# Kernel tuning notes

Hardware: AMD Instinct MI355X
Metric: run time of the kernel (lower is better)

The kernel has to match this reference:

```python
import jax, jax.numpy as jnp
import numpy as np

C_IN = 5
KERNEL = 4
DEPTH = 4
C = C_IN + 3  # original + time + 2 CNN channels


def conv1d(x, w, b):
    # x: (B, Cin, L), w: (Cout, Cin, K) -> (B, Cout, L-K+1), 'VALID' padding as in signatory.Augment defaults
    y = jax.lax.conv_general_dilated(x, w, (1,), 'VALID',
                                     dimension_numbers=('NCH', 'OIH', 'NCH'))
    return y + b[None, :, None]


def augment(inp, w1, b1, w2, b2, w3, b3):
    # inp: (B, L, C_in). Mirrors signatory.Augment with layer_sizes=(8,8,2), kernel_size=4,
    # include_original=True, include_time=True, activation=relu (between layers, not after last).
    B, L, _ = inp.shape
    trunc = KERNEL - 1
    orig = inp[:, trunc:, :]                                   # (B, L-3, C_in)
    time = jnp.linspace(0.0, 1.0, L, dtype=inp.dtype)[trunc:]  # time over original stream, truncated
    time = jnp.broadcast_to(time[None, :, None], (B, L - trunc, 1))
    h = conv1d(inp.transpose(0, 2, 1), w1, b1)   # (B, 8, L-3)
    h = conv1d(jax.nn.relu(h), w2, b2)           # (B, 8, L-3)
    h = conv1d(jax.nn.relu(h), w3, b3)           # (B, 2, L-3)
    return jnp.concatenate([orig, time, h.transpose(0, 2, 1)], axis=2)  # (B, L-3, C)


def signature(path):
    # Truncated path signature, depth 4, basepoint=True (zero basepoint prepended).
    # Chen's relation: sig <- sig (tensor) exp(dx), maintained as per-level tensors.
    B, S, Cc = path.shape
    base = jnp.zeros((B, 1, Cc), path.dtype)
    inc = jnp.diff(jnp.concatenate([base, path], axis=1), axis=1)  # (B, S, C) increments incl. basepoint
    inc = inc.transpose(1, 0, 2)  # (S, B, C) for scan

    def step(carry, dx):
        s1, s2, s3, s4 = carry
        # exp(dx) levels: dx^(k)/k!
        e1 = dx
        e2 = jnp.einsum('bi,bj->bij', dx, dx) / 2.0
        e3 = jnp.einsum('bij,bk->bijk', e2, dx) / 3.0
        e4 = jnp.einsum('bijk,bl->bijkl', e3, dx) / 4.0
        # Chen: (A (x) B)_k = sum_i A_i (x) B_{k-i}, A_0 = B_0 = 1
        n1 = s1 + e1
        n2 = s2 + e2 + jnp.einsum('bi,bj->bij', s1, e1)
        n3 = (s3 + e3 + jnp.einsum('bi,bjk->bijk', s1, e2)
              + jnp.einsum('bij,bk->bijk', s2, e1))
        n4 = (s4 + e4 + jnp.einsum('bi,bjkl->bijkl', s1, e3)
              + jnp.einsum('bij,bkl->bijkl', s2, e2)
              + jnp.einsum('bijk,bl->bijkl', s3, e1))
        return (n1, n2, n3, n4), None

    init = (jnp.zeros((B, Cc), path.dtype),
            jnp.zeros((B, Cc, Cc), path.dtype),
            jnp.zeros((B, Cc, Cc, Cc), path.dtype),
            jnp.zeros((B, Cc, Cc, Cc, Cc), path.dtype))
    (s1, s2, s3, s4), _ = jax.lax.scan(step, init, inc)
    return jnp.concatenate([s1.reshape(B, -1), s2.reshape(B, -1),
                            s3.reshape(B, -1), s4.reshape(B, -1)], axis=1)  # (B, 4680)


def setup_inputs() -> dict:
    key = jax.random.key(0)
    ks = jax.random.split(key, 4)
    B, L = 64, 256

    def init_conv(k, cout, cin, ksz):
        bound = 1.0 / np.sqrt(cin * ksz)
        kw, kb = jax.random.split(k)
        w = jax.random.uniform(kw, (cout, cin, ksz), jnp.float32, -bound, bound)
        b = jax.random.uniform(kb, (cout,), jnp.float32, -bound, bound)
        return w, b

    w1, b1 = init_conv(ks[1], 8, C_IN, KERNEL)
    w2, b2 = init_conv(ks[2], 8, 8, 1)
    w3, b3 = init_conv(ks[3], 2, 8, 1)
    inp = jax.random.normal(ks[0], (B, L, C_IN), jnp.float32)
    return {"inp": inp, "w1": w1, "b1": b1, "w2": w2, "b2": b2, "w3": w3, "b3": b3}


def reference(inp, w1, b1, w2, b2, w3, b3):
    x = augment(inp, w1, b1, w2, b2, w3, b3)  # (B, L-3, C)
    return signature(x)                       # (B, 4680)
```

## Files before the change

### kernel.cpp

```cpp
#include <hip/hip_runtime.h>

#define L_IN  256
#define CIN   5
#define SIG_N 4680

__global__ __launch_bounds__(512) void sig_fused_kernel(
    const float* __restrict__ inp,
    const float* __restrict__ w1, const float* __restrict__ b1,
    const float* __restrict__ w2, const float* __restrict__ b2,
    const float* __restrict__ w3, const float* __restrict__ b3,
    float* __restrict__ out)
{
    const int blk  = blockIdx.x;
    const int b    = blk >> 2;
    const int iq   = blk & 3;
    const int i0   = 2 * iq;
    const int tid  = threadIdx.x;
    const int w    = tid >> 6;
    const int lane = tid & 63;
    const int j    = lane >> 3;
    const int k    = lane & 7;

    __shared__ __align__(16) float dxs[264][8];
    __shared__ __align__(16) float sig3[8][592];
    __shared__ __align__(16) float s4red[8][1024];

    auto PI = [&](int x) {
        return (((x >> 1) == 0) | ((x >> 1) == iq)) ? (x ^ i0) : x;
    };

    const float* __restrict__ x = inp + b * (L_IN * CIN);
    float o[8];
    if (tid < 253) {
        float h1[8];
        #pragma unroll
        for (int q = 0; q < 8; ++q) h1[q] = b1[q];
        #pragma unroll
        for (int kk = 0; kk < 4; ++kk) {
            #pragma unroll
            for (int ci = 0; ci < CIN; ++ci) {
                float v = x[(tid + kk) * CIN + ci];
                #pragma unroll
                for (int q = 0; q < 8; ++q) h1[q] = fmaf(v, w1[q * 20 + ci * 4 + kk], h1[q]);
            }
        }
        float r1v[8];
        #pragma unroll
        for (int q = 0; q < 8; ++q) r1v[q] = h1[q] > 0.f ? h1[q] : 0.f;
        float h2[8];
        #pragma unroll
        for (int q = 0; q < 8; ++q) h2[q] = b2[q];
        #pragma unroll
        for (int p = 0; p < 8; ++p) {
            #pragma unroll
            for (int q = 0; q < 8; ++q) h2[q] = fmaf(r1v[p], w2[q * 8 + p], h2[q]);
        }
        float r2v[8];
        #pragma unroll
        for (int q = 0; q < 8; ++q) r2v[q] = h2[q] > 0.f ? h2[q] : 0.f;
        float h30 = b3[0], h31 = b3[1];
        #pragma unroll
        for (int p = 0; p < 8; ++p) {
            h30 = fmaf(r2v[p], w3[p], h30);
            h31 = fmaf(r2v[p], w3[8 + p], h31);
        }
        #pragma unroll
        for (int cc = 0; cc < 5; ++cc) o[cc] = x[(tid + 3) * CIN + cc];
        o[5] = (float)(tid + 3) * (1.0f / 255.0f);
        o[6] = h30;
        o[7] = h31;
    }
    if (tid < 88) dxs[253 + (tid >> 3)][tid & 7] = 0.f;
    if (tid < 253) {
        #pragma unroll
        for (int c = 0; c < 8; ++c) dxs[tid][PI(c)] = o[c];
    }
    __syncthreads();
    float curr[8], prevr[8];
    if (tid < 253) {
        #pragma unroll
        for (int ch = 0; ch < 8; ++ch) {
            curr[ch]  = dxs[tid][ch];
            prevr[ch] = (tid > 0) ? dxs[tid - 1][ch] : 0.f;
        }
    }
    __syncthreads();
    if (tid < 253) {
        #pragma unroll
        for (int ch = 0; ch < 8; ++ch) dxs[tid][ch] = curr[ch] - prevr[ch];
    }
    __syncthreads();

    const int rbase = w * 32;
    float t1[8], t2r[8], t3r[8];
    float s4v[2][8];
    #pragma unroll
    for (int i = 0; i < 8; ++i) { t1[i] = 0.f; t2r[i] = 0.f; t3r[i] = 0.f; }
    #pragma unroll
    for (int m = 0; m < 2; ++m)
        #pragma unroll
        for (int l = 0; l < 8; ++l) s4v[m][l] = 0.f;

    const float4* __restrict__ dx4 = reinterpret_cast<const float4*>(&dxs[0][0]);
    float own_p[2], bb_p[2];
    float4 r0_p[2], r1_p[2];
    #pragma unroll
    for (int u = 0; u < 2; ++u) {
        own_p[u] = dxs[rbase + u][k];
        bb_p[u]  = dxs[rbase + u][j];
        r0_p[u]  = dx4[2 * (rbase + u)];
        r1_p[u]  = dx4[2 * (rbase + u) + 1];
    }

    for (int tb = 0; tb < 32; tb += 2) {
        #pragma unroll
        for (int u = 0; u < 2; ++u) {
            const int tn = rbase + tb + u + 2;
            float  own_n = dxs[tn][k];
            float  bb_n  = dxs[tn][j];
            float4 r0_n  = dx4[2 * tn];
            float4 r1_n  = dx4[2 * tn + 1];

            const float own = own_p[u];
            const float bb  = bb_p[u];
            const float4 r0 = r0_p[u];
            const float4 r1 = r1_p[u];
            const float rr[8] = { r0.x, r0.y, r0.z, r0.w, r1.x, r1.y, r1.z, r1.w };

            const float c4_0 = fmaf(own, fmaf(bb, fmaf(t1[0], (1.0f / 6.0f),
                                r0.x * (1.0f / 24.0f)), 0.5f * t2r[0]), t3r[0]);
            const float c4_1 = fmaf(own, fmaf(bb, fmaf(t1[1], (1.0f / 6.0f),
                                r0.y * (1.0f / 24.0f)), 0.5f * t2r[1]), t3r[1]);
            #pragma unroll
            for (int l = 0; l < 8; ++l) {
                s4v[0][l] = fmaf(c4_0, rr[l], s4v[0][l]);
                s4v[1][l] = fmaf(c4_1, rr[l], s4v[1][l]);
            }

            #pragma unroll
            for (int i = 0; i < 8; ++i) {
                const float a  = rr[i];
                const float c3 = fmaf(bb, fmaf(t1[i], 0.5f, a * (1.0f / 6.0f)), t2r[i]);
                t3r[i] = fmaf(c3, own, t3r[i]);
                t2r[i] = fmaf(fmaf(a, 0.5f, t1[i]), bb, t2r[i]);
                t1[i] += a;
            }

            own_p[u] = own_n; bb_p[u] = bb_n;
            r0_p[u] = r0_n;   r1_p[u] = r1_n;
        }
    }

    if (lane == 0) {
        #pragma unroll
        for (int i = 0; i < 8; ++i) sig3[w][i] = t1[i];
    }
    if (k == 0) {
        #pragma unroll
        for (int i = 0; i < 8; ++i) sig3[w][8 + i * 8 + j] = t2r[i];
    }
    #pragma unroll
    for (int i = 0; i < 8; ++i) sig3[w][72 + (i * 8 + j) * 8 + k] = t3r[i];
    __syncthreads();

    float p1[2] = {0.f, 0.f}, p2[2] = {0.f, 0.f}, p3[2] = {0.f, 0.f};

    auto combine = [&](int cc) {
        const float* __restrict__ lp = sig3[cc];
        const float s1j  = lp[j];
        const float s1k  = lp[k];
        const float s2jk = lp[8 + j * 8 + k];
        #pragma unroll
        for (int m = 0; m < 2; ++m) {
            const float s1i  = lp[m];
            const float s2ij = lp[8 + m * 8 + j];
            const float s3i  = lp[72 + (m * 8 + j) * 8 + k];
            const float np3 = p3[m] + s3i + p1[m] * s2jk + p2[m] * s1k;
            const float np2 = p2[m] + s2ij + p1[m] * s1j;
            p3[m] = np3; p2[m] = np2; p1[m] += s1i;
        }
    };

    for (int cc = 0; cc < w; ++cc) combine(cc);
    {
        const float* __restrict__ lp = sig3[w];
        const float4 s1a = *reinterpret_cast<const float4*>(lp);
        const float4 s1b = *reinterpret_cast<const float4*>(lp + 4);
        const float4 s2a = *reinterpret_cast<const float4*>(lp + 8 + k * 8);
        const float4 s2b = *reinterpret_cast<const float4*>(lp + 8 + k * 8 + 4);
        const float4 s3a = *reinterpret_cast<const float4*>(lp + 72 + (j * 8 + k) * 8);
        const float4 s3b = *reinterpret_cast<const float4*>(lp + 72 + (j * 8 + k) * 8 + 4);
        const float s1r[8] = { s1a.x, s1a.y, s1a.z, s1a.w, s1b.x, s1b.y, s1b.z, s1b.w };
        const float s2r[8] = { s2a.x, s2a.y, s2a.z, s2a.w, s2b.x, s2b.y, s2b.z, s2b.w };
        const float s3r[8] = { s3a.x, s3a.y, s3a.z, s3a.w, s3b.x, s3b.y, s3b.z, s3b.w };
        #pragma unroll
        for (int m = 0; m < 2; ++m)
            #pragma unroll
            for (int l = 0; l < 8; ++l)
                s4v[m][l] = fmaf(p1[m], s3r[l],
                             fmaf(p2[m], s2r[l],
                              fmaf(p3[m], s1r[l], s4v[m][l])));
    }

    float* __restrict__ ob = out + (size_t)b * SIG_N;
    if (w == 7) {
        combine(7);
        const int pj = PI(j);
        const int pk = PI(k);
        #pragma unroll
        for (int m = 0; m < 2; ++m) {
            const int i = i0 + m;
            if (lane == 0) ob[i] = p1[m];
            if (k == 0)    ob[8 + i * 8 + pj] = p2[m];
            ob[72 + (i * 8 + pj) * 8 + pk] = p3[m];
        }
    }

    {
        float4* wp0 = reinterpret_cast<float4*>(&s4red[w][lane * 8]);
        wp0[0] = make_float4(s4v[0][0], s4v[0][1], s4v[0][2], s4v[0][3]);
        wp0[1] = make_float4(s4v[0][4], s4v[0][5], s4v[0][6], s4v[0][7]);
        float4* wp1 = reinterpret_cast<float4*>(&s4red[w][512 + lane * 8]);
        wp1[0] = make_float4(s4v[1][0], s4v[1][1], s4v[1][2], s4v[1][3]);
        wp1[1] = make_float4(s4v[1][4], s4v[1][5], s4v[1][6], s4v[1][7]);
    }
    __syncthreads();

    {
        const int m  = tid >> 8;
        const int jk = (tid >> 2) & 63;
        const int l0 = (tid & 3) << 1;
        const int off = m * 512 + jk * 8 + l0;
        float2 v; v.x = 0.f; v.y = 0.f;
        #pragma unroll
        for (int ww = 0; ww < 8; ++ww) {
            const float2 t = *reinterpret_cast<const float2*>(&s4red[ww][off]);
            v.x += t.x; v.y += t.y;
        }
        const int jp = jk >> 3, kp = jk & 7;
        const int gj = PI(jp);
        const int gk = PI(kp);
        const int gl = PI(l0);
        *reinterpret_cast<float2*>(ob + 584 + (i0 + m) * 512 + gj * 64 + gk * 8 + gl) = v;
    }
}

extern "C" void kernel_launch(void* const* d_in, const int* in_sizes, int n_in,
                              void* d_out, int out_size, void* d_ws, size_t ws_size,
                              hipStream_t stream)
{
    const float* inp = (const float*)d_in[0];
    const float* w1  = (const float*)d_in[1];
    const float* b1  = (const float*)d_in[2];
    const float* w2  = (const float*)d_in[3];
    const float* b2  = (const float*)d_in[4];
    const float* w3  = (const float*)d_in[5];
    const float* b3  = (const float*)d_in[6];
    float* out = (float*)d_out;

    sig_fused_kernel<<<256, 512, 0, stream>>>(inp, w1, b1, w2, b2, w3, b3, out);
}
```

Before: 78.91 us.

## Split work into one block per first signature index, doubling grid size

```diff
diff --git a/kernel.cpp b/kernel.cpp
--- a/kernel.cpp
+++ b/kernel.cpp
@@ -4,7 +4,7 @@
 #define CIN   5
 #define SIG_N 4680
 
-__global__ __launch_bounds__(512) void sig_fused_kernel(
+__global__ __launch_bounds__(512, 4) void sig_fused_kernel(
     const float* __restrict__ inp,
     const float* __restrict__ w1, const float* __restrict__ b1,
     const float* __restrict__ w2, const float* __restrict__ b2,
@@ -12,9 +12,8 @@
     float* __restrict__ out)
 {
     const int blk  = blockIdx.x;
-    const int b    = blk >> 2;
-    const int iq   = blk & 3;
-    const int i0   = 2 * iq;
+    const int b    = blk >> 3;
+    const int i    = blk & 7;
     const int tid  = threadIdx.x;
     const int w    = tid >> 6;
     const int lane = tid & 63;
@@ -23,11 +22,9 @@
 
     __shared__ __align__(16) float dxs[264][8];
     __shared__ __align__(16) float sig3[8][592];
-    __shared__ __align__(16) float s4red[8][1024];
-
-    auto PI = [&](int x) {
-        return (((x >> 1) == 0) | ((x >> 1) == iq)) ? (x ^ i0) : x;
-    };
+    __shared__ __align__(16) float s4red[8][512];
+
+    auto PI = [&](int x) { return (x == 0 || x == i) ? (x ^ i) : x; };
 
     const float* __restrict__ x = inp + b * (L_IN * CIN);
     float o[8];
@@ -93,13 +90,9 @@
 
     const int rbase = w * 32;
     float t1[8], t2r[8], t3r[8];
-    float s4v[2][8];
+    float s4v[8];
     #pragma unroll
-    for (int i = 0; i < 8; ++i) { t1[i] = 0.f; t2r[i] = 0.f; t3r[i] = 0.f; }
-    #pragma unroll
-    for (int m = 0; m < 2; ++m)
-        #pragma unroll
-        for (int l = 0; l < 8; ++l) s4v[m][l] = 0.f;
+    for (int q = 0; q < 8; ++q) { t1[q] = 0.f; t2r[q] = 0.f; t3r[q] = 0.f; s4v[q] = 0.f; }
 
     const float4* __restrict__ dx4 = reinterpret_cast<const float4*>(&dxs[0][0]);
     float own_p[2], bb_p[2];
@@ -127,23 +120,18 @@
             const float4 r1 = r1_p[u];
             const float rr[8] = { r0.x, r0.y, r0.z, r0.w, r1.x, r1.y, r1.z, r1.w };
 
-            const float c4_0 = fmaf(own, fmaf(bb, fmaf(t1[0], (1.0f / 6.0f),
-                                r0.x * (1.0f / 24.0f)), 0.5f * t2r[0]), t3r[0]);
-            const float c4_1 = fmaf(own, fmaf(bb, fmaf(t1[1], (1.0f / 6.0f),
-                                r0.y * (1.0f / 24.0f)), 0.5f * t2r[1]), t3r[1]);
-            #pragma unroll
-            for (int l = 0; l < 8; ++l) {
-                s4v[0][l] = fmaf(c4_0, rr[l], s4v[0][l]);
-                s4v[1][l] = fmaf(c4_1, rr[l], s4v[1][l]);
-            }
-
-            #pragma unroll
-            for (int i = 0; i < 8; ++i) {
-                const float a  = rr[i];
-                const float c3 = fmaf(bb, fmaf(t1[i], 0.5f, a * (1.0f / 6.0f)), t2r[i]);
-                t3r[i] = fmaf(c3, own, t3r[i]);
-                t2r[i] = fmaf(fmaf(a, 0.5f, t1[i]), bb, t2r[i]);
-                t1[i] += a;
+            const float c4 = fmaf(own, fmaf(bb, fmaf(t1[0], (1.0f / 6.0f),
+                               r0.x * (1.0f / 24.0f)), 0.5f * t2r[0]), t3r[0]);
+            #pragma unroll
+            for (int l = 0; l < 8; ++l) s4v[l] = fmaf(c4, rr[l], s4v[l]);
+
+            #pragma unroll
+            for (int q = 0; q < 8; ++q) {
+                const float a  = rr[q];
+                const float c3 = fmaf(bb, fmaf(t1[q], 0.5f, a * (1.0f / 6.0f)), t2r[q]);
+                t3r[q] = fmaf(c3, own, t3r[q]);
+                t2r[q] = fmaf(fmaf(a, 0.5f, t1[q]), bb, t2r[q]);
+                t1[q] += a;
             }
 
             own_p[u] = own_n; bb_p[u] = bb_n;
@@ -153,32 +141,29 @@
 
     if (lane == 0) {
         #pragma unroll
-        for (int i = 0; i < 8; ++i) sig3[w][i] = t1[i];
+        for (int q = 0; q < 8; ++q) sig3[w][q] = t1[q];
     }
     if (k == 0) {
         #pragma unroll
-        for (int i = 0; i < 8; ++i) sig3[w][8 + i * 8 + j] = t2r[i];
+        for (int q = 0; q < 8; ++q) sig3[w][8 + q * 8 + j] = t2r[q];
     }
     #pragma unroll
-    for (int i = 0; i < 8; ++i) sig3[w][72 + (i * 8 + j) * 8 + k] = t3r[i];
-    __syncthreads();
-
-    float p1[2] = {0.f, 0.f}, p2[2] = {0.f, 0.f}, p3[2] = {0.f, 0.f};
+    for (int q = 0; q < 8; ++q) sig3[w][72 + (q * 8 + j) * 8 + k] = t3r[q];
+    __syncthreads();
+
+    float p1 = 0.f, p2 = 0.f, p3 = 0.f;
 
     auto combine = [&](int cc) {
         const float* __restrict__ lp = sig3[cc];
         const float s1j  = lp[j];
         const float s1k  = lp[k];
         const float s2jk = lp[8 + j * 8 + k];
-        #pragma unroll
-        for (int m = 0; m < 2; ++m) {
-            const float s1i  = lp[m];
-            const float s2ij = lp[8 + m * 8 + j];
-            const float s3i  = lp[72 + (m * 8 + j) * 8 + k];
-            const float np3 = p3[m] + s3i + p1[m] * s2jk + p2[m] * s1k;
-            const float np2 = p2[m] + s2ij + p1[m] * s1j;
-            p3[m] = np3; p2[m] = np2; p1[m] += s1i;
-        }
+        const float s1i  = lp[0];
+        const float s2ij = lp[8 + j];
+        const float s3i  = lp[72 + j * 8 + k];
+        const float np3 = p3 + s3i + p1 * s2jk + p2 * s1k;
+        const float np2 = p2 + s2ij + p1 * s1j;
+        p3 = np3; p2 = np2; p1 += s1i;
     };
 
     for (int cc = 0; cc < w; ++cc) combine(cc);
@@ -194,12 +179,10 @@
         const float s2r[8] = { s2a.x, s2a.y, s2a.z, s2a.w, s2b.x, s2b.y, s2b.z, s2b.w };
         const float s3r[8] = { s3a.x, s3a.y, s3a.z, s3a.w, s3b.x, s3b.y, s3b.z, s3b.w };
         #pragma unroll
-        for (int m = 0; m < 2; ++m)
-            #pragma unroll
-            for (int l = 0; l < 8; ++l)
-                s4v[m][l] = fmaf(p1[m], s3r[l],
-                             fmaf(p2[m], s2r[l],
-                              fmaf(p3[m], s1r[l], s4v[m][l])));
+        for (int l = 0; l < 8; ++l)
+            s4v[l] = fmaf(p1, s3r[l],
+                      fmaf(p2, s2r[l],
+                       fmaf(p3, s1r[l], s4v[l])));
     }
 
     float* __restrict__ ob = out + (size_t)b * SIG_N;
@@ -207,41 +190,29 @@
         combine(7);
         const int pj = PI(j);
         const int pk = PI(k);
-        #pragma unroll
-        for (int m = 0; m < 2; ++m) {
-            const int i = i0 + m;
-            if (lane == 0) ob[i] = p1[m];
-            if (k == 0)    ob[8 + i * 8 + pj] = p2[m];
-            ob[72 + (i * 8 + pj) * 8 + pk] = p3[m];
-        }
+        if (lane == 0) ob[i] = p1;
+        if (k == 0)    ob[8 + i * 8 + pj] = p2;
+        ob[72 + (i * 8 + pj) * 8 + pk] = p3;
     }
 
     {
-        float4* wp0 = reinterpret_cast<float4*>(&s4red[w][lane * 8]);
-        wp0[0] = make_float4(s4v[0][0], s4v[0][1], s4v[0][2], s4v[0][3]);
-        wp0[1] = make_float4(s4v[0][4], s4v[0][5], s4v[0][6], s4v[0][7]);
-        float4* wp1 = reinterpret_cast<float4*>(&s4red[w][512 + lane * 8]);
-        wp1[0] = make_float4(s4v[1][0], s4v[1][1], s4v[1][2], s4v[1][3]);
-        wp1[1] = make_float4(s4v[1][4], s4v[1][5], s4v[1][6], s4v[1][7]);
+        float4* wp = reinterpret_cast<float4*>(&s4red[w][lane * 8]);
+        wp[0] = make_float4(s4v[0], s4v[1], s4v[2], s4v[3]);
+        wp[1] = make_float4(s4v[4], s4v[5], s4v[6], s4v[7]);
     }
     __syncthreads();
 
     {
-        const int m  = tid >> 8;
-        const int jk = (tid >> 2) & 63;
-        const int l0 = (tid & 3) << 1;
-        const int off = m * 512 + jk * 8 + l0;
-        float2 v; v.x = 0.f; v.y = 0.f;
-        #pragma unroll
-        for (int ww = 0; ww < 8; ++ww) {
-            const float2 t = *reinterpret_cast<const float2*>(&s4red[ww][off]);
-            v.x += t.x; v.y += t.y;
-        }
-        const int jp = jk >> 3, kp = jk & 7;
+        float v = 0.f;
+        #pragma unroll
+        for (int ww = 0; ww < 8; ++ww) v += s4red[ww][tid];
+        const int jp  = tid >> 6;
+        const int kp  = (tid >> 3) & 7;
+        const int lp2 = tid & 7;
         const int gj = PI(jp);
         const int gk = PI(kp);
-        const int gl = PI(l0);
-        *reinterpret_cast<float2*>(ob + 584 + (i0 + m) * 512 + gj * 64 + gk * 8 + gl) = v;
+        const int gl = PI(lp2);
+        ob[584 + i * 512 + gj * 64 + gk * 8 + gl] = v;
     }
 }
 
@@ -258,5 +229,5 @@
     const float* b3  = (const float*)d_in[6];
     float* out = (float*)d_out;
 
-    sig_fused_kernel<<<256, 512, 0, stream>>>(inp, w1, b1, w2, b2, w3, b3, out);
+    sig_fused_kernel<<<512, 512, 0, stream>>>(inp, w1, b1, w2, b2, w3, b3, out);
 }
```

After: 82.16 us. 4.1% more time.
